# Optimization experiments

Hardware: AMD Instinct MI355X
Metric: run time of the kernel (lower is better)

Reference implementation:

```python
import jax, jax.numpy as jnp
import numpy as np

B, L, D = 4096, 200, 64


def setup_inputs() -> dict:
    key = jax.random.key(0)
    ks = jax.random.split(key, 7)
    target_key = jax.random.normal(ks[0], (B, D), dtype=jnp.float32)
    item_keys = jax.random.normal(ks[1], (B, L, D), dtype=jnp.float32)
    item_values = jax.random.normal(ks[2], (B, L, D), dtype=jnp.float32)
    mask = jax.random.randint(ks[3], (B, L), 0, 2, dtype=jnp.int32)
    # Linear(D, D, bias=False) weights; torch applies y = x @ W.T
    scale = 1.0 / np.sqrt(D)
    W_target = jax.random.uniform(ks[4], (D, D), jnp.float32, -scale, scale)
    W_item = jax.random.uniform(ks[5], (D, D), jnp.float32, -scale, scale)
    W_value = jax.random.uniform(ks[6], (D, D), jnp.float32, -scale, scale)
    return {
        "target_key": target_key,
        "item_keys": item_keys,
        "item_values": item_values,
        "mask": mask,
        "W_target": W_target,
        "W_item": W_item,
        "W_value": W_value,
    }


def reference(target_key, item_keys, item_values, mask, W_target, W_item, W_value):
    scaler = jnp.float32(D) ** 0.5
    q = target_key @ W_target.T                      # [B, D]
    k = jnp.einsum("bld,ed->ble", item_keys, W_item)   # [B, L, D]
    v = jnp.einsum("bld,ed->ble", item_values, W_value) # [B, L, D]
    # single-query scores: broadcast multiply + reduce over D
    scores = jnp.einsum("bd,bld->bl", q, k) / scaler  # [B, L]
    scores = scores + (-1e8) * (1.0 - mask.astype(scores.dtype))
    w = jax.nn.softmax(scores, axis=1)                # softmax over L
    return jnp.einsum("bl,bld->bd", w, v)             # [B, D]
```

## Files before the change

### kernel.cpp

```cpp
#include <hip/hip_runtime.h>


#define B_ 4096
#define L_ 200
#define D_ 64

__global__ __launch_bounds__(256) void ta_kernel(
    const float* __restrict__ tk,
    const float* __restrict__ ik,
    const float* __restrict__ iv,
    const int*   __restrict__ mask,
    const float* __restrict__ Wt,
    const float* __restrict__ Wi,
    const float* __restrict__ Wv,
    float* __restrict__ out)
{
  const int t = threadIdx.x;
  const int b = blockIdx.x;

  __shared__ float q_s[D_];
  __shared__ float qt_s[D_];
  __shared__ float sc[L_];
  __shared__ float red[8];
  __shared__ float vred[256 * 4];
  __shared__ float sv[D_];

  if (t < D_) {
    const float* tkb = tk + (size_t)b * D_;
    float a = 0.f;
#pragma unroll
    for (int d = 0; d < D_; ++d) a += tkb[d] * Wt[t * D_ + d];
    q_s[t] = a;
  }
  __syncthreads();
  if (t < D_) {
    float a = 0.f;
#pragma unroll
    for (int e = 0; e < D_; ++e) a += q_s[e] * Wi[e * D_ + t];
    qt_s[t] = a;
  }
  __syncthreads();

  const float4* ik4 = (const float4*)(ik + (size_t)b * (L_ * D_));
  const float4* q4  = (const float4*)qt_s;
  if (t < L_) {
    float p = 0.f;
#pragma unroll
    for (int j = 0; j < 16; ++j) {
      float4 kv = ik4[t * 16 + j];
      float4 qq = q4[j];
      p += kv.x * qq.x + kv.y * qq.y + kv.z * qq.z + kv.w * qq.w;
    }
    float m = (float)mask[(size_t)b * L_ + t];
    sc[t] = p * 0.125f - 1e8f * (1.0f - m);
  }
  __syncthreads();

  float v = (t < L_) ? sc[t] : -3.0e38f;
#pragma unroll
  for (int off = 32; off >= 1; off >>= 1)
    v = fmaxf(v, __shfl_xor(v, off, 64));
  if ((t & 63) == 0) red[t >> 6] = v;
  __syncthreads();
  float mx = fmaxf(fmaxf(red[0], red[1]), fmaxf(red[2], red[3]));
  float ex = (t < L_) ? expf(sc[t] - mx) : 0.f;
  float s = ex;
#pragma unroll
  for (int off = 32; off >= 1; off >>= 1)
    s += __shfl_xor(s, off, 64);
  if ((t & 63) == 0) red[4 + (t >> 6)] = s;
  __syncthreads();
  float tot = red[4] + red[5] + red[6] + red[7];
  if (t < L_) sc[t] = ex / tot;
  __syncthreads();

  const float4* iv4 = (const float4*)(iv + (size_t)b * (L_ * D_));
  const int c = t & 15;
  const int rg = t >> 4;
  float4 acc = make_float4(0.f, 0.f, 0.f, 0.f);
#pragma unroll
  for (int it = 0; it < 13; ++it) {
    int row = it * 16 + rg;
    if (row < L_) {
      float w = sc[row];
      float4 vv = iv4[row * 16 + c];
      acc.x += w * vv.x; acc.y += w * vv.y;
      acc.z += w * vv.z; acc.w += w * vv.w;
    }
  }
  ((float4*)vred)[t] = acc;
  __syncthreads();
  if (t < D_) {
    float a = 0.f;
#pragma unroll
    for (int rg2 = 0; rg2 < 16; ++rg2) a += vred[rg2 * 64 + t];
    sv[t] = a;
  }
  __syncthreads();

  if (t < D_) {
    const float4* Wv4 = (const float4*)Wv;
    const float4* sv4 = (const float4*)sv;
    float a = 0.f;
#pragma unroll
    for (int cc = 0; cc < 16; ++cc) {
      float4 w4 = Wv4[t * 16 + cc];
      float4 s4 = sv4[cc];
      a += w4.x * s4.x + w4.y * s4.y + w4.z * s4.z + w4.w * s4.w;
    }
    out[(size_t)b * D_ + t] = a;
  }
}

extern "C" void kernel_launch(void* const* d_in, const int* in_sizes, int n_in,
                              void* d_out, int out_size, void* d_ws, size_t ws_size,
                              hipStream_t stream) {
  const float* tk   = (const float*)d_in[0];
  const float* ik   = (const float*)d_in[1];
  const float* iv   = (const float*)d_in[2];
  const int*   mask = (const int*)  d_in[3];
  const float* Wt   = (const float*)d_in[4];
  const float* Wi   = (const float*)d_in[5];
  const float* Wv   = (const float*)d_in[6];
  float* out = (float*)d_out;

  ta_kernel<<<B_, 256, 0, stream>>>(tk, ik, iv, mask, Wt, Wi, Wv, out);
}
```

Measured before the change: 427.2 us.

## Coalesce item_keys loads with 16-lane row groups and shuffle reductions

The key-score phase used to have each thread read one full 256-byte row, so a wavefront's accesses were strided. It now uses the same layout as the value pass: 16 threads cover one row with float4 loads, giving contiguous accesses across the wavefront, and the partial dot products are summed with xor shuffles. The mask is turned into an additive bias in shared memory at kernel start, and the target-key projection now uses float4 loads. The change adds shuffle work and a 13-iteration loop that all threads run.

```diff
diff --git a/kernel.cpp b/kernel.cpp
--- a/kernel.cpp
+++ b/kernel.cpp
@@ -17,19 +17,32 @@
 {
   const int t = threadIdx.x;
   const int b = blockIdx.x;
+  const int c  = t & 15;
+  const int rg = t >> 4;
 
   __shared__ float q_s[D_];
   __shared__ float qt_s[D_];
+  __shared__ float bias_s[L_];
   __shared__ float sc[L_];
   __shared__ float red[8];
   __shared__ float vred[256 * 4];
   __shared__ float sv[D_];
 
+  if (t < L_) {
+    int m = mask[(size_t)b * L_ + t];
+    bias_s[t] = m ? 0.0f : -1e8f;
+  }
+
   if (t < D_) {
-    const float* tkb = tk + (size_t)b * D_;
+    const float4* tkb4 = (const float4*)(tk + (size_t)b * D_);
+    const float4* Wt4  = (const float4*)Wt;
     float a = 0.f;
 #pragma unroll
-    for (int d = 0; d < D_; ++d) a += tkb[d] * Wt[t * D_ + d];
+    for (int j = 0; j < 16; ++j) {
+      float4 w = Wt4[t * 16 + j];
+      float4 x = tkb4[j];
+      a += w.x * x.x + w.y * x.y + w.z * x.z + w.w * x.w;
+    }
     q_s[t] = a;
   }
   __syncthreads();
@@ -43,16 +56,20 @@
 
   const float4* ik4 = (const float4*)(ik + (size_t)b * (L_ * D_));
   const float4* q4  = (const float4*)qt_s;
-  if (t < L_) {
+  const float4 qc = q4[c];
+#pragma unroll
+  for (int it = 0; it < 13; ++it) {
+    int row = it * 16 + rg;
     float p = 0.f;
-#pragma unroll
-    for (int j = 0; j < 16; ++j) {
-      float4 kv = ik4[t * 16 + j];
-      float4 qq = q4[j];
-      p += kv.x * qq.x + kv.y * qq.y + kv.z * qq.z + kv.w * qq.w;
+    if (row < L_) {
+      float4 kv = ik4[it * 256 + t];
+      p = kv.x * qc.x + kv.y * qc.y + kv.z * qc.z + kv.w * qc.w;
     }
-    float m = (float)mask[(size_t)b * L_ + t];
-    sc[t] = p * 0.125f - 1e8f * (1.0f - m);
+    p += __shfl_xor(p, 8, 64);
+    p += __shfl_xor(p, 4, 64);
+    p += __shfl_xor(p, 2, 64);
+    p += __shfl_xor(p, 1, 64);
+    if (c == 0 && row < L_) sc[row] = p * 0.125f + bias_s[row];
   }
   __syncthreads();
 
@@ -75,15 +92,13 @@
   __syncthreads();
 
   const float4* iv4 = (const float4*)(iv + (size_t)b * (L_ * D_));
-  const int c = t & 15;
-  const int rg = t >> 4;
   float4 acc = make_float4(0.f, 0.f, 0.f, 0.f);
 #pragma unroll
   for (int it = 0; it < 13; ++it) {
     int row = it * 16 + rg;
     if (row < L_) {
       float w = sc[row];
-      float4 vv = iv4[row * 16 + c];
+      float4 vv = iv4[it * 256 + t];
       acc.x += w * vv.x; acc.y += w * vv.y;
       acc.z += w * vv.z; acc.w += w * vv.w;
     }
```

Result: no change. 431.0 us (+0.9%).
